# Kernel tuning notes

Hardware: AMD Instinct MI355X
Metric: run time of the kernel (lower is better)

The kernel has to match this reference:

```python
import jax, jax.numpy as jnp
import numpy as np

D = 2048        # d_model
H = 16          # n_heads
HKV = 4         # n_kv_heads
DH = 128        # d_head = D // H
FF = int(D * 8 / 3)  # 5461, SwiGLU hidden
EPS = 1e-6
ROPE_BASE = 10000.0
B, L = 2, 2048


def rmsnorm(x, w):
    rms = jnp.sqrt(jnp.mean(x * x, axis=-1, keepdims=True) + EPS)
    return x / rms * w


def rope_cos_sin(seq_len):
    inv_freq = 1.0 / (ROPE_BASE ** (jnp.arange(0, DH, 2, dtype=jnp.float32) / DH))
    t = jnp.arange(seq_len, dtype=jnp.float32)
    freqs = t[:, None] * inv_freq[None, :]              # (L, DH/2)
    emb = jnp.concatenate([freqs, freqs], axis=-1)      # (L, DH)
    return jnp.cos(emb), jnp.sin(emb)


def rotate_half(x):
    x1, x2 = jnp.split(x, 2, axis=-1)
    return jnp.concatenate([-x2, x1], axis=-1)


def setup_inputs() -> dict:
    key = jax.random.key(0)
    ks = jax.random.split(key, 10)
    s = 0.02
    return {
        "x": jax.random.normal(ks[0], (B, L, D), dtype=jnp.float32),
        "w_norm1": jnp.ones((D,), dtype=jnp.float32),
        "wq": jax.random.normal(ks[1], (D, H * DH), dtype=jnp.float32) * s,
        "wk": jax.random.normal(ks[2], (D, HKV * DH), dtype=jnp.float32) * s,
        "wv": jax.random.normal(ks[3], (D, HKV * DH), dtype=jnp.float32) * s,
        "wo": jax.random.normal(ks[4], (H * DH, D), dtype=jnp.float32) * s,
        "w_norm2": jnp.ones((D,), dtype=jnp.float32),
        "w_gate": jax.random.normal(ks[5], (D, FF), dtype=jnp.float32) * s,
        "w_up": jax.random.normal(ks[6], (D, FF), dtype=jnp.float32) * s,
        "w_down": jax.random.normal(ks[7], (FF, D), dtype=jnp.float32) * s,
    }


def reference(x, w_norm1, wq, wk, wv, wo, w_norm2, w_gate, w_up, w_down):
    b, l, d = x.shape
    n_rep = H // HKV
    residual = x
    h = rmsnorm(x, w_norm1)
    q = (h @ wq).reshape(b, l, H, DH).transpose(0, 2, 1, 3)    # (B,H,L,DH)
    k = (h @ wk).reshape(b, l, HKV, DH).transpose(0, 2, 1, 3)  # (B,HKV,L,DH)
    v = (h @ wv).reshape(b, l, HKV, DH).transpose(0, 2, 1, 3)
    cos, sin = rope_cos_sin(l)                                 # (L,DH), broadcasts
    q = q * cos + rotate_half(q) * sin
    k = k * cos + rotate_half(k) * sin
    # GQA: repeat KV heads to match Q heads
    k = jnp.repeat(k, n_rep, axis=1)
    v = jnp.repeat(v, n_rep, axis=1)
    scale = 1.0 / np.sqrt(DH)
    attn = jnp.einsum('bhld,bhmd->bhlm', q, k) * scale         # (B,H,L,L)
    causal = jnp.triu(jnp.ones((l, l), dtype=bool), 1)
    attn = jnp.where(causal, -1e9, attn)
    attn = jax.nn.softmax(attn, axis=-1)
    out = jnp.einsum('bhlm,bhmd->bhld', attn, v)
    out = out.transpose(0, 2, 1, 3).reshape(b, l, d)
    x = residual + out @ wo
    residual = x
    h = rmsnorm(x, w_norm2)
    ffn = (jax.nn.silu(h @ w_gate) * (h @ w_up)) @ w_down
    return residual + ffn
```

## Files before the change

### kernel.cpp

```cpp
#include <hip/hip_runtime.h>
#include <stdint.h>

#define BATCH 2
#define SEQ   2048
#define DM    2048
#define NH    16
#define NKV   4
#define DHD   128
#define FFR   5461
#define FFP   5504
#define NTOK  (BATCH*SEQ)
#define QKVW  3072

typedef float f32x4 __attribute__((ext_vector_type(4)));
typedef short bf8v __attribute__((ext_vector_type(8)));
typedef unsigned short us8 __attribute__((ext_vector_type(8)));

__device__ __forceinline__ unsigned short f2bf(float f) {
  unsigned u = __float_as_uint(f);
  u += 0x7fff + ((u >> 16) & 1);
  return (unsigned short)(u >> 16);
}
__device__ __forceinline__ float bf2f(unsigned short b) {
  return __uint_as_float(((unsigned)b) << 16);
}

__device__ __forceinline__ void gload16(const void* g, void* l) {
  __builtin_amdgcn_global_load_lds(
      (const __attribute__((address_space(1))) unsigned int*)(uintptr_t)g,
      (__attribute__((address_space(3))) unsigned int*)(uintptr_t)l,
      16, 0, 0);
}

__global__ __launch_bounds__(256) void k_transpose(const float* __restrict__ S,
    unsigned short* __restrict__ T, int K, int N, int Kpad)
{
  __shared__ float tile[32][33];
  const int n0 = blockIdx.x << 5, k0 = blockIdx.y << 5;
  const int c = threadIdx.x & 31, r0 = threadIdx.x >> 5;
#pragma unroll
  for (int i = 0; i < 4; ++i) {
    int r = r0 + (i << 3);
    float v = 0.f;
    if ((k0 + r) < K && (n0 + c) < N) v = S[(long)(k0 + r) * N + n0 + c];
    tile[r][c] = v;
  }
  __syncthreads();
#pragma unroll
  for (int i = 0; i < 4; ++i) {
    int rr = r0 + (i << 3);
    T[(long)(n0 + rr) * Kpad + k0 + c] = f2bf(tile[c][rr]);
  }
}

__global__ __launch_bounds__(256) void k_transpose_v(const unsigned short* __restrict__ KV,
    unsigned short* __restrict__ VT)
{
  __shared__ unsigned short tile[32][36];
  const int kv0 = blockIdx.x << 5, d0 = blockIdx.y << 5;
  const int bz = blockIdx.z;
  const int b = bz >> 2, hkv = bz & 3;
  const int flat = threadIdx.x * 4;
  const int r = flat >> 5, c = flat & 31;
  ushort4 v = *(const ushort4*)(KV + ((long)(b*SEQ + kv0 + r))*QKVW + 2560 + hkv*128 + d0 + c);
  tile[r][c] = v.x; tile[r][c+1] = v.y; tile[r][c+2] = v.z; tile[r][c+3] = v.w;
  __syncthreads();
  ushort4 o;
  o.x = tile[c][r]; o.y = tile[c+1][r]; o.z = tile[c+2][r]; o.w = tile[c+3][r];
  *(ushort4*)(VT + ((long)(bz*128 + d0 + r))*SEQ + kv0 + c) = o;
}

__global__ __launch_bounds__(256) void k_rmsnorm(const float* __restrict__ X,
    const float* __restrict__ W, unsigned short* __restrict__ H)
{
  __shared__ float red[4];
  const long row = blockIdx.x;
  const float* xr = X + row * DM;
  const int tid = threadIdx.x;
  float4 a0 = ((const float4*)xr)[2*tid];
  float4 a1 = ((const float4*)xr)[2*tid+1];
  float ss = a0.x*a0.x + a0.y*a0.y + a0.z*a0.z + a0.w*a0.w
           + a1.x*a1.x + a1.y*a1.y + a1.z*a1.z + a1.w*a1.w;
#pragma unroll
  for (int m = 32; m >= 1; m >>= 1) ss += __shfl_xor(ss, m, 64);
  if ((tid & 63) == 0) red[tid >> 6] = ss;
  __syncthreads();
  float sc = rsqrtf((red[0]+red[1]+red[2]+red[3]) * (1.0f/DM) + 1e-6f);
  float4 w0 = ((const float4*)W)[2*tid];
  float4 w1 = ((const float4*)W)[2*tid+1];
  us8 o;
  o[0]=f2bf(a0.x*sc*w0.x); o[1]=f2bf(a0.y*sc*w0.y); o[2]=f2bf(a0.z*sc*w0.z); o[3]=f2bf(a0.w*sc*w0.w);
  o[4]=f2bf(a1.x*sc*w1.x); o[5]=f2bf(a1.y*sc*w1.y); o[6]=f2bf(a1.z*sc*w1.z); o[7]=f2bf(a1.w*sc*w1.w);
  *(us8*)(H + row*DM + tid*8) = o;
}

__global__ void k_rope_table(float* __restrict__ C, float* __restrict__ S)
{
  int i = blockIdx.x * 256 + threadIdx.x;
  int pos = i >> 6, d = i & 63;
  double inv = exp(-(double)d * (9.210340371976184 / 64.0));
  double ang = (double)pos * inv;
  C[i] = (float)cos(ang);
  S[i] = (float)sin(ang);
}

__global__ __launch_bounds__(256) void k_rope_apply(unsigned short* __restrict__ Q,
    const float* __restrict__ C, const float* __restrict__ S, int nh, int stride, int head0)
{
  long i = (long)blockIdx.x * 256 + threadIdx.x;
  int d = (int)(i & 63);
  long t = i >> 6;
  int hh = (int)(t % nh);
  long bl = t / nh;
  int pos = (int)(bl & (SEQ-1));
  long base = bl * stride + head0 + hh*DHD;
  float c = C[pos*64 + d], s = S[pos*64 + d];
  float x1 = bf2f(Q[base + d]);
  float x2 = bf2f(Q[base + 64 + d]);
  Q[base + d]      = f2bf(x1*c - x2*s);
  Q[base + 64 + d] = f2bf(x2*c + x1*s);
}

template<int EPI>
__global__ __launch_bounds__(256) void k_gemm(const unsigned short* __restrict__ A,
    const unsigned short* __restrict__ BT, void* Cout, const float* __restrict__ Res,
    const unsigned short* __restrict__ Gin, int K, int ldc)
{
  __shared__ __align__(16) unsigned short As[2][128*64];
  __shared__ __align__(16) unsigned short Bs[2][128*64];
  const int tid = threadIdx.x;
  const int l = tid & 63, w = tid >> 6;
  const int wr = w >> 1, wc = w & 1;
  const int nM = gridDim.x, nN = gridDim.y;
  const int nwg = nM * nN;
  const int bid = blockIdx.y * gridDim.x + blockIdx.x;
  const int q8 = nwg >> 3, r8 = nwg & 7, xcd = bid & 7, off8 = bid >> 3;
  const int wg = (xcd < r8 ? xcd*(q8+1) : r8*(q8+1) + (xcd - r8)*q8) + off8;
  const int colTiles = nM * 4;
  const int fullCols = nN >> 2, rem = nN & 3;
  int sc, inCol, wN;
  if (wg < fullCols * colTiles) { sc = wg / colTiles; inCol = wg % colTiles; wN = 4; }
  else { sc = fullCols; inCol = wg - fullCols * colTiles; wN = rem; }
  const int perSuper = 2 * wN;
  const int sm = inCol / perSuper, t8 = inCol % perSuper;
  const long m0 = (long)(sm*2 + t8 / wN) * 128;
  const long n0 = (long)(sc*4 + t8 % wN) * 128;
  const char* Ab = (const char*)(A + m0 * (long)K);
  const char* Bb = (const char*)(BT + n0 * (long)K);
  f32x4 acc[4][4] = {};
  const long ldab = (long)K * 2;
  const int nk = K >> 6;
  const int srow = w*32 + (l >> 3);
  const int scol = ((l & 7) ^ (srow & 7)) * 16;
  auto STAGE = [&](int buf, int kt) {
    const long kb = (long)kt * 128;
#pragma unroll
    for (int i = 0; i < 4; ++i) {
      gload16(Ab + (long)(srow + i*8)*ldab + kb + scol, &As[buf][(w*32 + i*8)*64]);
      gload16(Bb + (long)(srow + i*8)*ldab + kb + scol, &Bs[buf][(w*32 + i*8)*64]);
    }
  };
  STAGE(0, 0);
  __syncthreads();
  int cur = 0;
  for (int kt = 0; kt < nk; ++kt) {
    if (kt + 1 < nk) STAGE(cur ^ 1, kt + 1);
#pragma unroll
    for (int kk = 0; kk < 2; ++kk) {
      bf8v af[4], bfv[4];
#pragma unroll
      for (int m = 0; m < 4; ++m) {
        int r = wr*64 + m*16 + (l & 15);
        int offb = (kk*64 + (l >> 4)*16) ^ ((r & 7) << 4);
        af[m] = *(const bf8v*)((const char*)&As[cur][0] + r*128 + offb);
      }
#pragma unroll
      for (int n = 0; n < 4; ++n) {
        int cI = wc*64 + n*16 + (l & 15);
        int offb = (kk*64 + (l >> 4)*16) ^ ((cI & 7) << 4);
        bfv[n] = *(const bf8v*)((const char*)&Bs[cur][0] + cI*128 + offb);
      }
#pragma unroll
      for (int m = 0; m < 4; ++m)
#pragma unroll
        for (int n = 0; n < 4; ++n)
          acc[m][n] = __builtin_amdgcn_mfma_f32_16x16x32_bf16(af[m], bfv[n], acc[m][n], 0, 0, 0);
    }
    __syncthreads();
    cur ^= 1;
  }
#pragma unroll
  for (int m = 0; m < 4; ++m)
#pragma unroll
    for (int n = 0; n < 4; ++n)
#pragma unroll
      for (int r = 0; r < 4; ++r) {
        long row = m0 + wr*64 + m*16 + (l >> 4)*4 + r;
        long col = n0 + wc*64 + n*16 + (l & 15);
        long idx = row * (long)ldc + col;
        if (EPI == 0) ((unsigned short*)Cout)[idx] = f2bf(acc[m][n][r]);
        else if (EPI == 1) ((float*)Cout)[idx] = Res[idx] + acc[m][n][r];
        else {
          float g = bf2f(Gin[idx]);
          float sv = g / (1.f + __expf(-g));
          ((unsigned short*)Cout)[idx] = f2bf(sv * acc[m][n][r]);
        }
      }
}

__global__ __launch_bounds__(512) void k_attn(const unsigned short* __restrict__ QKV,
    const unsigned short* __restrict__ VbT, unsigned short* __restrict__ O)
{
  __shared__ __align__(16) unsigned short Ks[2][64*128];
  __shared__ __align__(16) unsigned short Vs[2][128*64];
  __shared__ __align__(16) unsigned short Pl[8][16][64];
  const int tid = threadIdx.x, l = tid & 63, w = tid >> 6;
  const int b = blockIdx.z, h = blockIdx.y;
  const int hkv = h >> 2;
  const float scale = 0.08838834764831845f;
  const unsigned short* Kbase = QKV + (long)b*SEQ*QKVW + 2048 + hkv*128;
  const unsigned short* Vtb = VbT + ((long)(b*NKV + hkv))*128*SEQ;

  for (int half = 0; half < 2; ++half) {
    const int qt = half ? (15 - (int)blockIdx.x) : (int)blockIdx.x;
    const int q0 = qt << 7;
    bf8v qa[4];
    {
      const unsigned short* qp = QKV + ((long)(b*SEQ + q0 + w*16 + (l & 15)))*QKVW + h*DHD + (l >> 4)*8;
#pragma unroll
      for (int kk = 0; kk < 4; ++kk) qa[kk] = *(const bf8v*)(qp + kk*32);
    }
    float m_[4], s_[4];
    f32x4 o_[8] = {};
#pragma unroll
    for (int r = 0; r < 4; ++r) { m_[r] = -1e30f; s_[r] = 0.f; }
    const int T = 2*qt + 2;
    const int qmaxw = q0 + w*16 + 15;

    auto STAGE = [&](int buf, int t) {
      const int kv0 = t << 6;
#pragma unroll
      for (int i = 0; i < 2; ++i) {
        int r = w*8 + i*4 + (l >> 4);
        int blk = (l & 15) ^ (r & 7);
        gload16(Kbase + ((long)(kv0 + r))*QKVW + blk*8, &Ks[buf][(w*8 + i*4)*128]);
      }
#pragma unroll
      for (int i = 0; i < 2; ++i) {
        int r = w*16 + i*8 + (l >> 3);
        int blk = (l & 7) ^ (r & 7);
        gload16(Vtb + (long)r*SEQ + kv0 + blk*8, &Vs[buf][(w*16 + i*8)*64]);
      }
    };
    STAGE(0, 0);
    __syncthreads();
    int cur = 0;
    for (int t = 0; t < T; ++t) {
      const int kv0 = t << 6;
      if (t + 1 < T) STAGE(cur ^ 1, t + 1);
      if (kv0 <= qmaxw) {
        f32x4 sc4[4] = {};
#pragma unroll
        for (int n = 0; n < 4; ++n) {
          int row = n*16 + (l & 15);
          const char* kr = (const char*)&Ks[cur][0] + row*256;
#pragma unroll
          for (int kk = 0; kk < 4; ++kk) {
            int off = (kk*64 + (l >> 4)*16) ^ ((row & 7) << 4);
            bf8v kf = *(const bf8v*)(kr + off);
            sc4[n] = __builtin_amdgcn_mfma_f32_16x16x32_bf16(qa[kk], kf, sc4[n], 0, 0, 0);
          }
        }
        float p[4][4];
        float rmax[4] = {-3e30f, -3e30f, -3e30f, -3e30f};
#pragma unroll
        for (int n = 0; n < 4; ++n) {
          int kv = kv0 + n*16 + (l & 15);
#pragma unroll
          for (int r = 0; r < 4; ++r) {
            int qr = q0 + w*16 + (l >> 4)*4 + r;
            float v = sc4[n][r] * scale;
            if (kv > qr) v = -1e30f;
            p[n][r] = v;
            rmax[r] = fmaxf(rmax[r], v);
          }
        }
#pragma unroll
        for (int r = 0; r < 4; ++r) {
          rmax[r] = fmaxf(rmax[r], __shfl_xor(rmax[r], 1, 64));
          rmax[r] = fmaxf(rmax[r], __shfl_xor(rmax[r], 2, 64));
          rmax[r] = fmaxf(rmax[r], __shfl_xor(rmax[r], 4, 64));
          rmax[r] = fmaxf(rmax[r], __shfl_xor(rmax[r], 8, 64));
        }
        float alpha[4], ps[4];
#pragma unroll
        for (int r = 0; r < 4; ++r) {
          float mn = fmaxf(m_[r], rmax[r]);
          alpha[r] = __expf(m_[r] - mn);
          m_[r] = mn;
          ps[r] = 0.f;
        }
#pragma unroll
        for (int n = 0; n < 4; ++n)
#pragma unroll
          for (int r = 0; r < 4; ++r) {
            float e = __expf(p[n][r] - m_[r]);
            p[n][r] = e;
            ps[r] += e;
          }
#pragma unroll
        for (int r = 0; r < 4; ++r) {
          ps[r] += __shfl_xor(ps[r], 1, 64);
          ps[r] += __shfl_xor(ps[r], 2, 64);
          ps[r] += __shfl_xor(ps[r], 4, 64);
          ps[r] += __shfl_xor(ps[r], 8, 64);
          s_[r] = s_[r]*alpha[r] + ps[r];
        }
#pragma unroll
        for (int g = 0; g < 8; ++g) {
          o_[g][0] *= alpha[0]; o_[g][1] *= alpha[1];
          o_[g][2] *= alpha[2]; o_[g][3] *= alpha[3];
        }
#pragma unroll
        for (int n = 0; n < 4; ++n)
#pragma unroll
          for (int r = 0; r < 4; ++r)
            Pl[w][(l >> 4)*4 + r][n*16 + (l & 15)] = f2bf(p[n][r]);
#pragma unroll
        for (int kk2 = 0; kk2 < 2; ++kk2) {
          bf8v pa = *(const bf8v*)&Pl[w][l & 15][kk2*32 + (l >> 4)*8];
#pragma unroll
          for (int g = 0; g < 8; ++g) {
            int d = g*16 + (l & 15);
            int off = (kk2*64 + (l >> 4)*16) ^ ((d & 7) << 4);
            bf8v vf = *(const bf8v*)((const char*)&Vs[cur][0] + d*128 + off);
            o_[g] = __builtin_amdgcn_mfma_f32_16x16x32_bf16(pa, vf, o_[g], 0, 0, 0);
          }
        }
      }
      __syncthreads();
      cur ^= 1;
    }
#pragma unroll
    for (int g = 0; g < 8; ++g)
#pragma unroll
      for (int r = 0; r < 4; ++r) {
        long row = (long)b*SEQ + q0 + w*16 + (l >> 4)*4 + r;
        O[row*DM + h*DHD + g*16 + (l & 15)] = f2bf(o_[g][r] / s_[r]);
      }
  }
}

extern "C" void kernel_launch(void* const* d_in, const int* in_sizes, int n_in,
                              void* d_out, int out_size, void* d_ws, size_t ws_size,
                              hipStream_t stream)
{
  const float* x   = (const float*)d_in[0];
  const float* wn1 = (const float*)d_in[1];
  const float* wq  = (const float*)d_in[2];
  const float* wk  = (const float*)d_in[3];
  const float* wv  = (const float*)d_in[4];
  const float* wo  = (const float*)d_in[5];
  const float* wn2 = (const float*)d_in[6];
  const float* wg  = (const float*)d_in[7];
  const float* wu  = (const float*)d_in[8];
  const float* wd  = (const float*)d_in[9];
  float* out = (float*)d_out;

  char* p = (char*)d_ws;
  auto alloc = [&](size_t bytes) { char* r = p; p += (bytes + 255) & ~(size_t)255; return r; };
  unsigned short* wqkvT = (unsigned short*)alloc((size_t)QKVW*2048*2);
  unsigned short* woT  = (unsigned short*)alloc((size_t)2048*2048*2);
  unsigned short* wgT  = (unsigned short*)alloc((size_t)FFP*2048*2);
  unsigned short* wuT  = (unsigned short*)alloc((size_t)FFP*2048*2);
  unsigned short* wdT  = (unsigned short*)alloc((size_t)2048*FFP*2);
  unsigned short* hb   = (unsigned short*)alloc((size_t)NTOK*2048*2);
  unsigned short* pr   = (unsigned short*)alloc((size_t)NTOK*FFP*2);
  char* scratch = p;
  unsigned short* qkv  = (unsigned short*)alloc((size_t)NTOK*QKVW*2);
  unsigned short* vbT  = (unsigned short*)alloc((size_t)BATCH*NKV*128*SEQ*2);
  unsigned short* ao   = (unsigned short*)alloc((size_t)NTOK*2048*2);
  float* ctab = (float*)alloc((size_t)SEQ*64*4);
  float* stab = (float*)alloc((size_t)SEQ*64*4);
  unsigned short* gb   = (unsigned short*)scratch;

  dim3 blk(256);
  k_transpose<<<dim3(2048/32, 2048/32), blk, 0, stream>>>(wq, wqkvT, 2048, 2048, 2048);
  k_transpose<<<dim3(512/32,  2048/32), blk, 0, stream>>>(wk, wqkvT + (size_t)2048*2048, 2048, 512, 2048);
  k_transpose<<<dim3(512/32,  2048/32), blk, 0, stream>>>(wv, wqkvT + (size_t)2560*2048, 2048, 512, 2048);
  k_transpose<<<dim3(2048/32, 2048/32), blk, 0, stream>>>(wo, woT, 2048, 2048, 2048);
  k_transpose<<<dim3(FFP/32,  2048/32), blk, 0, stream>>>(wg, wgT, 2048, FFR, 2048);
  k_transpose<<<dim3(FFP/32,  2048/32), blk, 0, stream>>>(wu, wuT, 2048, FFR, 2048);
  k_transpose<<<dim3(2048/32, FFP/32),  blk, 0, stream>>>(wd, wdT, FFR, 2048, FFP);

  k_rope_table<<<dim3(SEQ*64/256), blk, 0, stream>>>(ctab, stab);
  k_rmsnorm<<<dim3(NTOK), blk, 0, stream>>>(x, wn1, hb);

  k_gemm<0><<<dim3(32, QKVW/128), blk, 0, stream>>>(hb, wqkvT, qkv, nullptr, nullptr, 2048, QKVW);

  k_rope_apply<<<dim3(NTOK*NH*64/256),  blk, 0, stream>>>(qkv, ctab, stab, NH, QKVW, 0);
  k_rope_apply<<<dim3(NTOK*NKV*64/256), blk, 0, stream>>>(qkv, ctab, stab, NKV, QKVW, 2048);

  k_transpose_v<<<dim3(SEQ/32, 128/32, BATCH*NKV), blk, 0, stream>>>(qkv, vbT);

  k_attn<<<dim3(8, NH, BATCH), dim3(512), 0, stream>>>(qkv, vbT, ao);

  k_gemm<1><<<dim3(32, 16), blk, 0, stream>>>(ao, woT, (void*)out, x, nullptr, 2048, 2048);
  k_rmsnorm<<<dim3(NTOK), blk, 0, stream>>>(out, wn2, hb);
  k_gemm<0><<<dim3(32, FFP/128), blk, 0, stream>>>(hb, wgT, gb, nullptr, nullptr, 2048, FFP);
  k_gemm<2><<<dim3(32, FFP/128), blk, 0, stream>>>(hb, wuT, pr, nullptr, gb, 2048, FFP);
  k_gemm<1><<<dim3(32, 16), blk, 0, stream>>>(pr, wdT, (void*)out, out, nullptr, FFP, 2048);
}
```

Measured before the change: 692.0 us.

## Switch GEMM to single-buffered K=32 tiles with packed swizzled LDS layout

The GEMM kernel drops the double-buffered 128x64 LDS tiles in favour of a single 128x32 buffer per operand, loaded and consumed each K step with two barriers. Rows are packed in pairs into 128-byte LDS lines with an XOR swizzle, so each fragment read is one 16-byte load. This cuts LDS use roughly fourfold, which may allow more workgroups per CU. In exchange it loses the overlap between global prefetch and MFMA work and doubles the number of loop iterations and barriers.

```diff
diff --git a/kernel.cpp b/kernel.cpp
--- a/kernel.cpp
+++ b/kernel.cpp
@@ -122,15 +122,15 @@
 }
 
 template<int EPI>
-__global__ __launch_bounds__(256) void k_gemm(const unsigned short* __restrict__ A,
+__global__ __launch_bounds__(256) void k_gemm97(const unsigned short* __restrict__ A,
     const unsigned short* __restrict__ BT, void* Cout, const float* __restrict__ Res,
     const unsigned short* __restrict__ Gin, int K, int ldc)
 {
-  __shared__ __align__(16) unsigned short As[2][128*64];
-  __shared__ __align__(16) unsigned short Bs[2][128*64];
-  const int tid = threadIdx.x;
-  const int l = tid & 63, w = tid >> 6;
+  __shared__ __align__(16) unsigned short As[64][64];
+  __shared__ __align__(16) unsigned short Bs[64][64];
+  const int tid = threadIdx.x, l = tid & 63, w = tid >> 6;
   const int wr = w >> 1, wc = w & 1;
+  const int la = l & 15, q = l >> 4;
   const int nM = gridDim.x, nN = gridDim.y;
   const int nwg = nM * nN;
   const int bid = blockIdx.y * gridDim.x + blockIdx.x;
@@ -138,65 +138,58 @@
   const int wg = (xcd < r8 ? xcd*(q8+1) : r8*(q8+1) + (xcd - r8)*q8) + off8;
   const int colTiles = nM * 4;
   const int fullCols = nN >> 2, rem = nN & 3;
-  int sc, inCol, wN;
-  if (wg < fullCols * colTiles) { sc = wg / colTiles; inCol = wg % colTiles; wN = 4; }
-  else { sc = fullCols; inCol = wg - fullCols * colTiles; wN = rem; }
+  int sc_, inCol, wN;
+  if (wg < fullCols * colTiles) { sc_ = wg / colTiles; inCol = wg % colTiles; wN = 4; }
+  else { sc_ = fullCols; inCol = wg - fullCols * colTiles; wN = rem; }
   const int perSuper = 2 * wN;
   const int sm = inCol / perSuper, t8 = inCol % perSuper;
   const long m0 = (long)(sm*2 + t8 / wN) * 128;
-  const long n0 = (long)(sc*4 + t8 % wN) * 128;
+  const long n0 = (long)(sc_*4 + t8 % wN) * 128;
   const char* Ab = (const char*)(A + m0 * (long)K);
   const char* Bb = (const char*)(BT + n0 * (long)K);
+  const long ldab = (long)K * 2;
+  const int nk = K >> 5;
+  const int srp = tid >> 3;
+  const int ssl = tid & 7;
+  const int fOff = (la >> 1)*128 + (((((la & 1) << 2) + q) ^ ((la >> 1) & 7)) << 4);
+
   f32x4 acc[4][4] = {};
-  const long ldab = (long)K * 2;
-  const int nk = K >> 6;
-  const int srow = w*32 + (l >> 3);
-  const int scol = ((l & 7) ^ (srow & 7)) * 16;
-  auto STAGE = [&](int buf, int kt) {
-    const long kb = (long)kt * 128;
-#pragma unroll
-    for (int i = 0; i < 4; ++i) {
-      gload16(Ab + (long)(srow + i*8)*ldab + kb + scol, &As[buf][(w*32 + i*8)*64]);
-      gload16(Bb + (long)(srow + i*8)*ldab + kb + scol, &Bs[buf][(w*32 + i*8)*64]);
-    }
-  };
-  STAGE(0, 0);
-  __syncthreads();
-  int cur = 0;
+
   for (int kt = 0; kt < nk; ++kt) {
-    if (kt + 1 < nk) STAGE(cur ^ 1, kt + 1);
-#pragma unroll
-    for (int kk = 0; kk < 2; ++kk) {
-      bf8v af[4], bfv[4];
-#pragma unroll
-      for (int m = 0; m < 4; ++m) {
-        int r = wr*64 + m*16 + (l & 15);
-        int offb = (kk*64 + (l >> 4)*16) ^ ((r & 7) << 4);
-        af[m] = *(const bf8v*)((const char*)&As[cur][0] + r*128 + offb);
-      }
-#pragma unroll
-      for (int n = 0; n < 4; ++n) {
-        int cI = wc*64 + n*16 + (l & 15);
-        int offb = (kk*64 + (l >> 4)*16) ^ ((cI & 7) << 4);
-        bfv[n] = *(const bf8v*)((const char*)&Bs[cur][0] + cI*128 + offb);
-      }
-#pragma unroll
-      for (int m = 0; m < 4; ++m)
-#pragma unroll
-        for (int n = 0; n < 4; ++n)
-          acc[m][n] = __builtin_amdgcn_mfma_f32_16x16x32_bf16(af[m], bfv[n], acc[m][n], 0, 0, 0);
+    const long kb = (long)kt * 64;
+#pragma unroll
+    for (int i = 0; i < 2; ++i) {
+      int rp = i*32 + srp;
+      int bs = ssl ^ (rp & 7);
+      long grow = 2*rp + (bs >> 2);
+      long goff = grow*ldab + kb + (long)(bs & 3)*16;
+      gload16(Ab + goff, (char*)As + i*4096 + tid*16);
+      gload16(Bb + goff, (char*)Bs + i*4096 + tid*16);
     }
     __syncthreads();
-    cur ^= 1;
+    bf8v af[4], bfv[4];
+#pragma unroll
+    for (int m = 0; m < 4; ++m)
+      af[m] = *(const bf8v*)((const char*)As + wr*4096 + m*1024 + fOff);
+#pragma unroll
+    for (int n = 0; n < 4; ++n)
+      bfv[n] = *(const bf8v*)((const char*)Bs + wc*4096 + n*1024 + fOff);
+#pragma unroll
+    for (int m = 0; m < 4; ++m)
+#pragma unroll
+      for (int n = 0; n < 4; ++n)
+        acc[m][n] = __builtin_amdgcn_mfma_f32_16x16x32_bf16(af[m], bfv[n], acc[m][n], 0, 0, 0);
+    __syncthreads();
   }
+
 #pragma unroll
   for (int m = 0; m < 4; ++m)
 #pragma unroll
     for (int n = 0; n < 4; ++n)
 #pragma unroll
       for (int r = 0; r < 4; ++r) {
-        long row = m0 + wr*64 + m*16 + (l >> 4)*4 + r;
-        long col = n0 + wc*64 + n*16 + (l & 15);
+        long row = m0 + wr*64 + m*16 + q*4 + r;
+        long col = n0 + wc*64 + n*16 + la;
         long idx = row * (long)ldc + col;
         if (EPI == 0) ((unsigned short*)Cout)[idx] = f2bf(acc[m][n][r]);
         else if (EPI == 1) ((float*)Cout)[idx] = Res[idx] + acc[m][n][r];
@@ -396,7 +389,7 @@
   k_rope_table<<<dim3(SEQ*64/256), blk, 0, stream>>>(ctab, stab);
   k_rmsnorm<<<dim3(NTOK), blk, 0, stream>>>(x, wn1, hb);
 
-  k_gemm<0><<<dim3(32, QKVW/128), blk, 0, stream>>>(hb, wqkvT, qkv, nullptr, nullptr, 2048, QKVW);
+  k_gemm97<0><<<dim3(32, QKVW/128), blk, 0, stream>>>(hb, wqkvT, qkv, nullptr, nullptr, 2048, QKVW);
 
   k_rope_apply<<<dim3(NTOK*NH*64/256),  blk, 0, stream>>>(qkv, ctab, stab, NH, QKVW, 0);
   k_rope_apply<<<dim3(NTOK*NKV*64/256), blk, 0, stream>>>(qkv, ctab, stab, NKV, QKVW, 2048);
@@ -405,9 +398,9 @@
 
   k_attn<<<dim3(8, NH, BATCH), dim3(512), 0, stream>>>(qkv, vbT, ao);
 
-  k_gemm<1><<<dim3(32, 16), blk, 0, stream>>>(ao, woT, (void*)out, x, nullptr, 2048, 2048);
+  k_gemm97<1><<<dim3(32, 16), blk, 0, stream>>>(ao, woT, (void*)out, x, nullptr, 2048, 2048);
   k_rmsnorm<<<dim3(NTOK), blk, 0, stream>>>(out, wn2, hb);
-  k_gemm<0><<<dim3(32, FFP/128), blk, 0, stream>>>(hb, wgT, gb, nullptr, nullptr, 2048, FFP);
-  k_gemm<2><<<dim3(32, FFP/128), blk, 0, stream>>>(hb, wuT, pr, nullptr, gb, 2048, FFP);
-  k_gemm<1><<<dim3(32, 16), blk, 0, stream>>>(pr, wdT, (void*)out, out, nullptr, FFP, 2048);
-}
+  k_gemm97<0><<<dim3(32, FFP/128), blk, 0, stream>>>(hb, wgT, gb, nullptr, nullptr, 2048, FFP);
+  k_gemm97<2><<<dim3(32, FFP/128), blk, 0, stream>>>(hb, wuT, pr, nullptr, gb, 2048, FFP);
+  k_gemm97<1><<<dim3(32, 16), blk, 0, stream>>>(pr, wdT, (void*)out, out, nullptr, FFP, 2048);
+}
```

New measurement: 813.5 us. 1.18x slower.

## Fuse gate and up GEMMs via interleaved weight layout; add setprio in attention

Applied to the files above, without the earlier changes.

The gate and up weight matrices are transposed into one interleaved buffer in which each 64-column output tile holds alternating 16-row blocks of gate and up. A single GEMM then computes both, and its epilogue applies SiLU(gate)*up directly, so the gate intermediate is never written to or read back from global memory and one launch is removed. Separately, the attention kernel raises wave priority around its MFMA sections with s_setprio. The interleaved layout ties the epilogue's column mapping to a fixed warp tiling, which makes it fragile if tile sizes change.

```diff
diff --git a/kernel.cpp b/kernel.cpp
--- a/kernel.cpp
+++ b/kernel.cpp
@@ -50,6 +50,29 @@
   for (int i = 0; i < 4; ++i) {
     int rr = r0 + (i << 3);
     T[(long)(n0 + rr) * Kpad + k0 + c] = f2bf(tile[c][rr]);
+  }
+}
+
+__global__ __launch_bounds__(256) void k_transpose_fu(const float* __restrict__ S,
+    unsigned short* __restrict__ T, int K, int N, int Kpad, int m01)
+{
+  __shared__ float tile[32][33];
+  const int n0 = blockIdx.x << 5, k0 = blockIdx.y << 5;
+  const int c = threadIdx.x & 31, r0 = threadIdx.x >> 5;
+#pragma unroll
+  for (int i = 0; i < 4; ++i) {
+    int r = r0 + (i << 3);
+    float v = 0.f;
+    if ((k0 + r) < K && (n0 + c) < N) v = S[(long)(k0 + r) * N + n0 + c];
+    tile[r][c] = v;
+  }
+  __syncthreads();
+#pragma unroll
+  for (int i = 0; i < 4; ++i) {
+    int rr = r0 + (i << 3);
+    int n = n0 + rr;
+    long rp = (long)(n >> 6)*128 + ((n & 63) >> 4)*32 + m01*16 + (n & 15);
+    T[rp * Kpad + k0 + c] = f2bf(tile[c][rr]);
   }
 }
 
@@ -124,7 +147,7 @@
 template<int EPI>
 __global__ __launch_bounds__(256) void k_gemm(const unsigned short* __restrict__ A,
     const unsigned short* __restrict__ BT, void* Cout, const float* __restrict__ Res,
-    const unsigned short* __restrict__ Gin, int K, int ldc)
+    int K, int ldc)
 {
   __shared__ __align__(16) unsigned short As[2][128*64];
   __shared__ __align__(16) unsigned short Bs[2][128*64];
@@ -189,6 +212,21 @@
     __syncthreads();
     cur ^= 1;
   }
+  if (EPI == 3) {
+#pragma unroll
+    for (int m = 0; m < 4; ++m)
+#pragma unroll
+      for (int n = 0; n < 4; n += 2)
+#pragma unroll
+        for (int r = 0; r < 4; ++r) {
+          long row = m0 + wr*64 + m*16 + (l >> 4)*4 + r;
+          long col = (n0 >> 1) + (wc*2 + (n >> 1))*16 + (l & 15);
+          float g = acc[m][n][r], u = acc[m][n+1][r];
+          float sv = g / (1.f + __expf(-g));
+          ((unsigned short*)Cout)[row * (long)ldc + col] = f2bf(sv * u);
+        }
+    return;
+  }
 #pragma unroll
   for (int m = 0; m < 4; ++m)
 #pragma unroll
@@ -199,12 +237,7 @@
         long col = n0 + wc*64 + n*16 + (l & 15);
         long idx = row * (long)ldc + col;
         if (EPI == 0) ((unsigned short*)Cout)[idx] = f2bf(acc[m][n][r]);
-        else if (EPI == 1) ((float*)Cout)[idx] = Res[idx] + acc[m][n][r];
-        else {
-          float g = bf2f(Gin[idx]);
-          float sv = g / (1.f + __expf(-g));
-          ((unsigned short*)Cout)[idx] = f2bf(sv * acc[m][n][r]);
-        }
+        else          ((float*)Cout)[idx] = Res[idx] + acc[m][n][r];
       }
 }
 
@@ -260,6 +293,7 @@
       if (t + 1 < T) STAGE(cur ^ 1, t + 1);
       if (kv0 <= qmaxw) {
         f32x4 sc4[4] = {};
+        __builtin_amdgcn_s_setprio(1);
 #pragma unroll
         for (int n = 0; n < 4; ++n) {
           int row = n*16 + (l & 15);
@@ -271,6 +305,7 @@
             sc4[n] = __builtin_amdgcn_mfma_f32_16x16x32_bf16(qa[kk], kf, sc4[n], 0, 0, 0);
           }
         }
+        __builtin_amdgcn_s_setprio(0);
         float p[4][4];
         float rmax[4] = {-3e30f, -3e30f, -3e30f, -3e30f};
 #pragma unroll
@@ -326,6 +361,7 @@
 #pragma unroll
           for (int r = 0; r < 4; ++r)
             Pl[w][(l >> 4)*4 + r][n*16 + (l & 15)] = f2bf(p[n][r]);
+        __builtin_amdgcn_s_setprio(1);
 #pragma unroll
         for (int kk2 = 0; kk2 < 2; ++kk2) {
           bf8v pa = *(const bf8v*)&Pl[w][l & 15][kk2*32 + (l >> 4)*8];
@@ -337,6 +373,7 @@
             o_[g] = __builtin_amdgcn_mfma_f32_16x16x32_bf16(pa, vf, o_[g], 0, 0, 0);
           }
         }
+        __builtin_amdgcn_s_setprio(0);
       }
       __syncthreads();
       cur ^= 1;
@@ -370,33 +407,30 @@
   char* p = (char*)d_ws;
   auto alloc = [&](size_t bytes) { char* r = p; p += (bytes + 255) & ~(size_t)255; return r; };
   unsigned short* wqkvT = (unsigned short*)alloc((size_t)QKVW*2048*2);
-  unsigned short* woT  = (unsigned short*)alloc((size_t)2048*2048*2);
-  unsigned short* wgT  = (unsigned short*)alloc((size_t)FFP*2048*2);
-  unsigned short* wuT  = (unsigned short*)alloc((size_t)FFP*2048*2);
-  unsigned short* wdT  = (unsigned short*)alloc((size_t)2048*FFP*2);
-  unsigned short* hb   = (unsigned short*)alloc((size_t)NTOK*2048*2);
-  unsigned short* pr   = (unsigned short*)alloc((size_t)NTOK*FFP*2);
-  char* scratch = p;
-  unsigned short* qkv  = (unsigned short*)alloc((size_t)NTOK*QKVW*2);
-  unsigned short* vbT  = (unsigned short*)alloc((size_t)BATCH*NKV*128*SEQ*2);
-  unsigned short* ao   = (unsigned short*)alloc((size_t)NTOK*2048*2);
+  unsigned short* woT   = (unsigned short*)alloc((size_t)2048*2048*2);
+  unsigned short* wguT  = (unsigned short*)alloc((size_t)2*FFP*2048*2);
+  unsigned short* wdT   = (unsigned short*)alloc((size_t)2048*FFP*2);
+  unsigned short* hb    = (unsigned short*)alloc((size_t)NTOK*2048*2);
+  unsigned short* pr    = (unsigned short*)alloc((size_t)NTOK*FFP*2);
+  unsigned short* qkv   = (unsigned short*)alloc((size_t)NTOK*QKVW*2);
+  unsigned short* vbT   = (unsigned short*)alloc((size_t)BATCH*NKV*128*SEQ*2);
+  unsigned short* ao    = (unsigned short*)alloc((size_t)NTOK*2048*2);
   float* ctab = (float*)alloc((size_t)SEQ*64*4);
   float* stab = (float*)alloc((size_t)SEQ*64*4);
-  unsigned short* gb   = (unsigned short*)scratch;
 
   dim3 blk(256);
   k_transpose<<<dim3(2048/32, 2048/32), blk, 0, stream>>>(wq, wqkvT, 2048, 2048, 2048);
   k_transpose<<<dim3(512/32,  2048/32), blk, 0, stream>>>(wk, wqkvT + (size_t)2048*2048, 2048, 512, 2048);
   k_transpose<<<dim3(512/32,  2048/32), blk, 0, stream>>>(wv, wqkvT + (size_t)2560*2048, 2048, 512, 2048);
   k_transpose<<<dim3(2048/32, 2048/32), blk, 0, stream>>>(wo, woT, 2048, 2048, 2048);
-  k_transpose<<<dim3(FFP/32,  2048/32), blk, 0, stream>>>(wg, wgT, 2048, FFR, 2048);
-  k_transpose<<<dim3(FFP/32,  2048/32), blk, 0, stream>>>(wu, wuT, 2048, FFR, 2048);
+  k_transpose_fu<<<dim3(FFP/32, 2048/32), blk, 0, stream>>>(wg, wguT, 2048, FFR, 2048, 0);
+  k_transpose_fu<<<dim3(FFP/32, 2048/32), blk, 0, stream>>>(wu, wguT, 2048, FFR, 2048, 1);
   k_transpose<<<dim3(2048/32, FFP/32),  blk, 0, stream>>>(wd, wdT, FFR, 2048, FFP);
 
   k_rope_table<<<dim3(SEQ*64/256), blk, 0, stream>>>(ctab, stab);
   k_rmsnorm<<<dim3(NTOK), blk, 0, stream>>>(x, wn1, hb);
 
-  k_gemm<0><<<dim3(32, QKVW/128), blk, 0, stream>>>(hb, wqkvT, qkv, nullptr, nullptr, 2048, QKVW);
+  k_gemm<0><<<dim3(32, QKVW/128), blk, 0, stream>>>(hb, wqkvT, qkv, nullptr, 2048, QKVW);
 
   k_rope_apply<<<dim3(NTOK*NH*64/256),  blk, 0, stream>>>(qkv, ctab, stab, NH, QKVW, 0);
   k_rope_apply<<<dim3(NTOK*NKV*64/256), blk, 0, stream>>>(qkv, ctab, stab, NKV, QKVW, 2048);
@@ -405,9 +439,8 @@
 
   k_attn<<<dim3(8, NH, BATCH), dim3(512), 0, stream>>>(qkv, vbT, ao);
 
-  k_gemm<1><<<dim3(32, 16), blk, 0, stream>>>(ao, woT, (void*)out, x, nullptr, 2048, 2048);
+  k_gemm<1><<<dim3(32, 16), blk, 0, stream>>>(ao, woT, (void*)out, x, 2048, 2048);
   k_rmsnorm<<<dim3(NTOK), blk, 0, stream>>>(out, wn2, hb);
-  k_gemm<0><<<dim3(32, FFP/128), blk, 0, stream>>>(hb, wgT, gb, nullptr, nullptr, 2048, FFP);
-  k_gemm<2><<<dim3(32, FFP/128), blk, 0, stream>>>(hb, wuT, pr, nullptr, gb, 2048, FFP);
-  k_gemm<1><<<dim3(32, 16), blk, 0, stream>>>(pr, wdT, (void*)out, out, nullptr, FFP, 2048);
-}
+  k_gemm<3><<<dim3(32, 2*FFP/128), blk, 0, stream>>>(hb, wguT, pr, nullptr, 2048, FFP);
+  k_gemm<1><<<dim3(32, 16), blk, 0, stream>>>(pr, wdT, (void*)out, out, FFP, 2048);
+}
```

Measured after the change: 642.6 us. 7.1% less time.
